# Optimization experiments

Hardware: AMD Instinct MI355X
Metric: run time of the kernel (lower is better)

Reference implementation:

```python
import jax, jax.numpy as jnp
import numpy as np

B, S, D = 2, 2048, 1024
H, HD, R = 16, 64, 128
BLOCK, TOPK = 64, 4
ROPE_BASE = 100000.0
NEG = -1e30  # finite large-negative instead of -inf to avoid NaN rows


def _rope_tables(seq_len, dim, dtype):
    inv_freq = 1.0 / (ROPE_BASE ** (jnp.arange(0, dim, 2, dtype=jnp.float32) / dim))
    freqs = jnp.arange(seq_len, dtype=jnp.float32)[:, None] * inv_freq[None, :]  # [S, dim/2]
    emb = jnp.concatenate([freqs, freqs], axis=-1)  # [S, dim]
    return jnp.cos(emb).astype(dtype), jnp.sin(emb).astype(dtype)


def _rotate_half(t):
    t1, t2 = jnp.split(t, 2, axis=-1)
    return jnp.concatenate([-t2, t1], axis=-1)


def _apply_rope(t, cos, sin):
    # t: [B, H, S, HD]; cos/sin: [S, HD]
    return t * cos[None, None] + _rotate_half(t) * sin[None, None]


def setup_inputs() -> dict:
    key = jax.random.key(0)
    ks = jax.random.split(key, 6)
    s = 0.02
    return {
        "x": jax.random.normal(ks[0], (B, S, D), jnp.float32),
        "w_q": jax.random.normal(ks[1], (D, D), jnp.float32) * s,
        "w_kv_down": jax.random.normal(ks[2], (R, D), jnp.float32) * s,
        "w_kv_up": jax.random.normal(ks[3], (2 * D, R), jnp.float32) * s,
        "w_out": jax.random.normal(ks[4], (D, D), jnp.float32) * s,
        "w_scorer": jax.random.normal(ks[5], (1, D), jnp.float32) * s,
    }


def reference(x, w_q, w_kv_down, w_kv_up, w_out, w_scorer):
    b, s, d = x.shape
    nb = s // BLOCK  # S divisible by block_size here

    q = (x @ w_q.T).reshape(b, s, H, HD).transpose(0, 2, 1, 3)  # [B,H,S,HD]
    latent = x @ w_kv_down.T                                      # [B,S,R]
    kv = latent @ w_kv_up.T                                       # [B,S,2D]
    k, v = jnp.split(kv, 2, axis=-1)
    k = k.reshape(b, s, H, HD).transpose(0, 2, 1, 3)
    v = v.reshape(b, s, H, HD).transpose(0, 2, 1, 3)

    cos, sin = _rope_tables(s, HD, x.dtype)
    q = _apply_rope(q, cos, sin)
    k = _apply_rope(k, cos, sin)

    # block relevance scores from mean-pooled block reps of x
    block_reps = x.reshape(b, nb, BLOCK, d).mean(axis=2)          # [B,nb,D]
    block_scores = (block_reps @ w_scorer.T)[..., 0]              # [B,nb]
    _, top_idx = jax.lax.top_k(block_scores, min(TOPK, nb))       # [B,topk]

    # sparse key mask: True where key position lies in a selected block
    sel = jnp.zeros((b, nb), dtype=bool)
    sel = sel.at[jnp.arange(b)[:, None], top_idx].set(True)       # [B,nb]
    sparse_mask = jnp.repeat(sel, BLOCK, axis=1)                  # [B,S]

    causal = jnp.tril(jnp.ones((s, s), dtype=bool))               # True = allowed
    allowed = sparse_mask[:, None, None, :] & causal[None, None]  # [B,1,S,S]

    scale = 1.0 / jnp.sqrt(jnp.asarray(HD, x.dtype))
    scores = jnp.einsum("bhqd,bhkd->bhqk", q, k) * scale          # [B,H,S,S]
    scores = jnp.where(allowed, scores, NEG)
    attn = jax.nn.softmax(scores, axis=-1)
    out = jnp.einsum("bhqk,bhkd->bhqd", attn, v)                  # [B,H,S,HD]
    out = out.transpose(0, 2, 1, 3).reshape(b, s, d)
    return out @ w_out.T
```

## Files before the change

### kernel.cpp

```cpp
#include <hip/hip_runtime.h>
#include <hip/hip_bf16.h>
#include <math.h>

#define B_ 2
#define S_ 2048
#define D_ 1024
#define H_ 16
#define HD_ 64
#define R_ 128
#define NBLK 32
#define TOPK_ 4
#define BS_ (B_*S_)

typedef __attribute__((ext_vector_type(8))) short bf16x8;
typedef __attribute__((ext_vector_type(4))) float f32x4;

__device__ __forceinline__ unsigned short f2bf(float f) {
    unsigned int u = __float_as_uint(f);
    u += 0x7fffu + ((u >> 16) & 1u);
    return (unsigned short)(u >> 16);
}
__device__ __forceinline__ float bf2f(unsigned short h) {
    return __uint_as_float(((unsigned int)h) << 16);
}
__device__ __forceinline__ unsigned int pack2(float a, float b) {
    return (unsigned int)f2bf(a) | ((unsigned int)f2bf(b) << 16);
}
__device__ __forceinline__ void gload_lds16(const void* g, void* l) {
    __builtin_amdgcn_global_load_lds((const __attribute__((address_space(1))) void*)g,
                                     (__attribute__((address_space(3))) void*)l, 16, 0, 0);
}

__global__ __launch_bounds__(256) void prep_k(const float* __restrict__ x,
        const float* __restrict__ wsc, const float* __restrict__ wq,
        const float* __restrict__ wkd, const float* __restrict__ wku,
        const float* __restrict__ wo, float* __restrict__ cosT,
        float* __restrict__ sinT, unsigned short* __restrict__ wcat,
        unsigned short* __restrict__ wkub, unsigned short* __restrict__ wob,
        float* __restrict__ rows, unsigned short* __restrict__ xb) {
    const int blk = blockIdx.x;
    if (blk < 512) {
        const int idx = blk*256 + threadIdx.x;
        const int s  = idx >> 6;
        const int hd = idx & 63;
        const int j = (hd < 32) ? hd : hd - 32;
        const float inv = powf(100000.0f, -((float)(2*j) / 64.0f));
        const float fr = (float)s * inv;
        cosT[idx] = cosf(fr);
        sinT[idx] = sinf(fr);
    } else if (blk < 1728) {
        const int wb = blk - 512;
        const float* src; unsigned short* dst; int base;
        if      (wb < 512) { src = wq;  dst = wcat;            base = wb;       }
        else if (wb < 576) { src = wkd; dst = wcat + 1048576;  base = wb - 512; }
        else if (wb < 704) { src = wku; dst = wkub;            base = wb - 576; }
        else               { src = wo;  dst = wob;             base = wb - 704; }
        const int i = base*2048 + threadIdx.x*8;
        float4 a = *(const float4*)&src[i];
        float4 b = *(const float4*)&src[i+4];
        uint4 o;
        o.x = pack2(a.x, a.y); o.y = pack2(a.z, a.w);
        o.z = pack2(b.x, b.y); o.w = pack2(b.z, b.w);
        *(uint4*)&dst[i] = o;
    } else {
        const int wid  = ((blk - 1728) << 2) + (threadIdx.x >> 6);
        const int lane = threadIdx.x & 63;
        #pragma unroll
        for (int r = 0; r < 4; ++r) {
            const int row = (wid << 2) + r;
            const float* xp = x + (size_t)row * D_;
            unsigned short* xo = xb + (size_t)row * D_;
            float acc = 0.f;
            #pragma unroll
            for (int j = 0; j < 4; ++j) {
                const int off = ((j << 6) + lane) << 2;
                float4 xv = *(const float4*)&xp[off];
                float4 wv = *(const float4*)&wsc[off];
                acc = fmaf(xv.x, wv.x, acc);
                acc = fmaf(xv.y, wv.y, acc);
                acc = fmaf(xv.z, wv.z, acc);
                acc = fmaf(xv.w, wv.w, acc);
                uint2 o; o.x = pack2(xv.x, xv.y); o.y = pack2(xv.z, xv.w);
                *(uint2*)&xo[off] = o;
            }
            #pragma unroll
            for (int m = 1; m <= 32; m <<= 1) acc += __shfl_xor(acc, m);
            if (lane == 0) rows[row] = acc;
        }
    }
}

__global__ __launch_bounds__(256) void blocktopk_k(const float* __restrict__ rows,
        int* __restrict__ sel, float* __restrict__ vsum) {
    ((float4*)vsum)[threadIdx.x]       = (float4){0.f,0.f,0.f,0.f};
    ((float4*)vsum)[threadIdx.x + 256] = (float4){0.f,0.f,0.f,0.f};
    __shared__ float bs[64];
    const int bk = threadIdx.x >> 2, qt = threadIdx.x & 3;
    const float* rp = rows + (bk << 6) + (qt << 4);
    float p = 0.f;
    #pragma unroll
    for (int i = 0; i < 16; ++i) p += rp[i];
    p += __shfl_xor(p, 1);
    p += __shfl_xor(p, 2);
    if (qt == 0) bs[bk] = p;
    __syncthreads();
    if (threadIdx.x < B_) {
        const int b = threadIdx.x;
        float sc[NBLK];
        for (int i = 0; i < NBLK; ++i) sc[i] = bs[b * NBLK + i];
        for (int j = 0; j < TOPK_; ++j) {
            float best = -INFINITY; int bi = 0;
            for (int i = 0; i < NBLK; ++i)
                if (sc[i] > best) { best = sc[i]; bi = i; }
            sel[b * TOPK_ + j] = bi;
            sc[bi] = -INFINITY;
        }
    }
}

template<int EPI>
__global__ __launch_bounds__(256) void gemm_mfma_k(const unsigned short* __restrict__ A,
        const unsigned short* __restrict__ Bm, int M, int N, int K,
        void* __restrict__ o0, void* __restrict__ o1,
        const float* __restrict__ cosT, const float* __restrict__ sinT,
        float* __restrict__ vsum) {
    __shared__ unsigned short shbuf[2][12288];
    const int tid  = threadIdx.x;
    const int wave = tid >> 6, lane = tid & 63;
    const int nx = N >> 6;
    const int ob = blockIdx.x;
    const int w  = ((ob & 7) * (gridDim.x >> 3)) + (ob >> 3);
    const int bm = (w / nx) << 7, bn = (w % nx) << 6;
    const int g  = lane >> 4, qc = lane & 15;
    const int srow  = lane >> 3;
    const int sslot = (lane & 7) ^ srow;

    f32x4 acc[2][4];
    #pragma unroll
    for (int m=0;m<2;m++)
        #pragma unroll
        for (int n=0;n<4;n++)
            acc[m][n] = (f32x4){0.f,0.f,0.f,0.f};

    const int NT = K >> 6;
    auto STAGE = [&](int buf, int t) {
        const int k0 = t << 6;
        unsigned short* As = shbuf[buf];
        unsigned short* Bs = shbuf[buf] + 8192;
        #pragma unroll
        for (int it = 0; it < 4; ++it) {
            const int chunk = (it << 2) | wave;
            const int row   = (chunk << 3) | srow;
            gload_lds16(A + (size_t)(bm + row) * K + k0 + (sslot << 3), &As[chunk << 9]);
        }
        #pragma unroll
        for (int it = 0; it < 2; ++it) {
            const int chunk = (it << 2) | wave;
            const int row   = (chunk << 3) | srow;
            gload_lds16(Bm + (size_t)(bn + row) * K + k0 + (sslot << 3), &Bs[chunk << 9]);
        }
    };

    STAGE(0, 0);
    __syncthreads();
    for (int t = 0; t < NT; ++t) {
        if (t + 1 < NT) STAGE((t + 1) & 1, t + 1);
        const unsigned short* As = shbuf[t & 1];
        const unsigned short* Bs = shbuf[t & 1] + 8192;
        #pragma unroll
        for (int ks = 0; ks < 2; ++ks) {
            const int swb = ((ks << 2) | g) ^ (lane & 7);
            bf16x8 af[2], bfr[4];
            #pragma unroll
            for (int m = 0; m < 2; ++m)
                af[m]  = *(const bf16x8*)&As[(((wave << 5) + (m << 4) + qc) << 6) + (swb << 3)];
            #pragma unroll
            for (int n = 0; n < 4; ++n)
                bfr[n] = *(const bf16x8*)&Bs[(((n << 4) + qc) << 6) + (swb << 3)];
            #pragma unroll
            for (int m = 0; m < 2; ++m)
                #pragma unroll
                for (int n = 0; n < 4; ++n)
                    acc[m][n] = __builtin_amdgcn_mfma_f32_16x16x32_bf16(af[m], bfr[n], acc[m][n], 0, 0, 0);
        }
        __syncthreads();
    }

    if (EPI == 0) {
        float* C = (float*)o0;
        #pragma unroll
        for (int m = 0; m < 2; ++m) {
            const int r0 = bm + (wave << 5) + (m << 4) + (g << 2);
            #pragma unroll
            for (int n = 0; n < 4; ++n) {
                const int c = bn + (n << 4) + qc;
                #pragma unroll
                for (int j = 0; j < 4; ++j)
                    C[(size_t)(r0 + j) * N + c] = acc[m][n][j];
            }
        }
    } else {
        const bool isrope = (bn < 1024);
        if (isrope) {
            const int h = bn >> 6;
            unsigned short* dst = (unsigned short*)o0;
            #pragma unroll
            for (int m = 0; m < 2; ++m) {
                const int r0 = bm + (wave << 5) + (m << 4) + (g << 2);
                #pragma unroll
                for (int j = 0; j < 4; ++j) {
                    const int row = r0 + j;
                    const int b = row >> 11, s = row & (S_-1);
                    const size_t obase = ((size_t)(b*H_ + h) * S_ + s) << 6;
                    #pragma unroll
                    for (int n = 0; n < 4; ++n) {
                        const int hd = (n << 4) + qc;
                        const float c_ = cosT[(s << 6) + hd];
                        const float sn = sinT[(s << 6) + hd];
                        const float rot = (n < 2) ? -acc[m][n ^ 2][j] : acc[m][n ^ 2][j];
                        dst[obase + hd] = f2bf(acc[m][n][j] * c_ + rot * sn);
                    }
                }
            }
        } else if (EPI == 1) {
            unsigned short* latb = (unsigned short*)o1;
            const int c0 = bn - 1024;
            #pragma unroll
            for (int m = 0; m < 2; ++m) {
                const int r0 = bm + (wave << 5) + (m << 4) + (g << 2);
                #pragma unroll
                for (int n = 0; n < 4; ++n) {
                    const int c = c0 + (n << 4) + qc;
                    #pragma unroll
                    for (int j = 0; j < 4; ++j)
                        latb[(size_t)(r0 + j) * R_ + c] = f2bf(acc[m][n][j]);
                }
            }
        } else {
            const int h  = (bn >> 6) - 16;
            const int b  = bm >> 11, s0 = bm & (S_-1);
            const int bh = (b << 4) + h;
            unsigned short* vtb = (unsigned short*)o1;
            unsigned short (*T)[72] = (unsigned short(*)[72])&shbuf[0][0];
            #pragma unroll
            for (int m = 0; m < 2; ++m) {
                const int r0 = (wave << 5) + (m << 4) + (g << 2);
                #pragma unroll
                for (int n = 0; n < 4; ++n)
                    #pragma unroll
                    for (int j = 0; j < 4; ++j)
                        T[r0 + j][(n << 4) + qc] = f2bf(acc[m][n][j]);
            }
            __syncthreads();
            #pragma unroll
            for (int u = 0; u < 2; ++u) {
                const int kb = (s0 >> 6) + u;
                unsigned short* dst = vtb + (((size_t)(bh * NBLK + kb)) << 12);
                #pragma unroll
                for (int uu = 0; uu < 2; ++uu) {
                    const int idx = (uu << 8) + tid;
                    const int dd = idx >> 3, k0 = (idx & 7) << 3;
                    unsigned short tmp[8];
                    float sm = 0.f;
                    #pragma unroll
                    for (int j = 0; j < 8; ++j) { tmp[j] = T[(u << 6) + k0 + j][dd]; sm += bf2f(tmp[j]); }
                    *(uint4*)&dst[(size_t)(dd << 6) + k0] = *(uint4*)tmp;
                    sm += __shfl_xor(sm, 1);
                    sm += __shfl_xor(sm, 2);
                    sm += __shfl_xor(sm, 4);
                    if ((tid & 7) == 0) atomicAdd(&vsum[(bh << 6) + dd], sm);
                }
            }
        }
    }
}

__global__ __launch_bounds__(256) void attn_mfma_k(const unsigned short* __restrict__ qrb,
        const unsigned short* __restrict__ krb, const unsigned short* __restrict__ vtb,
        const int* __restrict__ sel, const float* __restrict__ vsum,
        unsigned short* __restrict__ attno) {
    const int qb = blockIdx.x & (NBLK-1);
    const int bh = blockIdx.x >> 5;
    const int b  = bh >> 4;
    const int h  = bh & 15;
    const int tid  = threadIdx.x;
    const int wave = tid >> 6, lane = tid & 63;
    const int g = lane >> 4, qc = lane & 15;

    __shared__ unsigned short Ks[64*64];
    __shared__ unsigned short Vt[64*64];
    __shared__ unsigned short Pl[4][16][72];
    __shared__ float cfl[4][16];
    __shared__ float lvl[4][16];

    int selb[4];
    #pragma unroll
    for (int j=0;j<4;j++) selb[j] = sel[(b<<2)+j];
    const bool diag = (selb[0]==qb)|(selb[1]==qb)|(selb[2]==qb)|(selb[3]==qb);

    int kbl[5]; int cnt = 0;
    #pragma unroll
    for (int j=0;j<4;j++) if (selb[j] < qb) kbl[cnt++] = selb[j];
    const int dstart = cnt;
    if (diag) kbl[cnt++] = qb;

    const unsigned short* qp = qrb + (((size_t)bh*S_ + (qb<<6) + (wave<<4) + qc) << 6);
    bf16x8 bq[2];
    bq[0] = *(const bf16x8*)(qp + (g<<3));
    bq[1] = *(const bf16x8*)(qp + 32 + (g<<3));

    f32x4 oacc[4];
    #pragma unroll
    for (int n=0;n<4;n++) oacc[n] = (f32x4){0.f,0.f,0.f,0.f};
    float mrun = -INFINITY, lrun = 0.f;
    const int qib = (wave<<4) + qc;

    const int srow = lane >> 3;
    const int sslot = (lane & 7) ^ srow;

    for (int i = 0; i < cnt; ++i) {
        const int kb = kbl[i];
        const bool isdiag = (i >= dstart);
        const unsigned short* kB = krb + (((size_t)bh*S_ + (kb<<6)) << 6);
        const unsigned short* vT = vtb + (((size_t)(bh*NBLK + kb)) << 12);
        __syncthreads();
        #pragma unroll
        for (int it = 0; it < 2; ++it) {
            const int chunk = (it << 2) | wave;
            const int row = (chunk << 3) | srow;
            gload_lds16(kB + (row << 6) + (sslot << 3), &Ks[chunk << 9]);
            gload_lds16(vT + (row << 6) + (sslot << 3), &Vt[chunk << 9]);
        }
        __syncthreads();

        f32x4 sf[4];
        #pragma unroll
        for (int m=0;m<4;m++) sf[m] = (f32x4){0.f,0.f,0.f,0.f};
        #pragma unroll
        for (int ks=0;ks<2;ks++)
            #pragma unroll
            for (int m=0;m<4;m++) {
                const int sw = (((ks<<2)|g) ^ (qc & 7)) << 3;
                bf16x8 ak = *(const bf16x8*)&Ks[(((m<<4)+qc)<<6) + sw];
                sf[m] = __builtin_amdgcn_mfma_f32_16x16x32_bf16(ak, bq[ks], sf[m], 0, 0, 0);
            }

        float s[16];
        float bmax = -INFINITY;
        #pragma unroll
        for (int m=0;m<4;m++)
            #pragma unroll
            for (int r2=0;r2<4;r2++) {
                const int kl = (m<<4)+(g<<2)+r2;
                float v = sf[m][r2]*0.125f;
                if (isdiag && kl > qib) v = -1e30f;
                s[(m<<2)+r2] = v;
                bmax = fmaxf(bmax, v);
            }
        bmax = fmaxf(bmax, __shfl_xor(bmax, 16));
        bmax = fmaxf(bmax, __shfl_xor(bmax, 32));
        const float mnew = fmaxf(mrun, bmax);
        const float cf = __expf(mrun - mnew);
        float ls = 0.f;
        #pragma unroll
        for (int m=0;m<4;m++) {
            float p0 = __expf(s[(m<<2)+0]-mnew);
            float p1 = __expf(s[(m<<2)+1]-mnew);
            float p2 = __expf(s[(m<<2)+2]-mnew);
            float p3 = __expf(s[(m<<2)+3]-mnew);
            ls += p0+p1+p2+p3;
            const int koff = (m<<4)+(g<<2);
            *(unsigned int*)&Pl[wave][qc][koff]   = pack2(p0,p1);
            *(unsigned int*)&Pl[wave][qc][koff+2] = pack2(p2,p3);
        }
        ls += __shfl_xor(ls, 16);
        ls += __shfl_xor(ls, 32);
        lrun = lrun*cf + ls;
        cfl[wave][qc] = cf;
        f32x4 cf4 = *(const f32x4*)&cfl[wave][g<<2];
        #pragma unroll
        for (int n=0;n<4;n++) oacc[n] *= cf4;
        #pragma unroll
        for (int ks=0;ks<2;ks++) {
            bf16x8 pa = *(const bf16x8*)&Pl[wave][qc][(ks<<5)+(g<<3)];
            #pragma unroll
            for (int n=0;n<4;n++) {
                const int sw = (((ks<<2)|g) ^ (qc & 7)) << 3;
                bf16x8 vb = *(const bf16x8*)&Vt[(((n<<4)+qc)<<6) + sw];
                oacc[n] = __builtin_amdgcn_mfma_f32_16x16x32_bf16(pa, vb, oacc[n], 0, 0, 0);
            }
        }
        mrun = mnew;
    }

    f32x4 il4 = (f32x4){0.f,0.f,0.f,0.f};
    if (cnt) {
        lvl[wave][qc] = 1.0f / lrun;
        il4 = *(const f32x4*)&lvl[wave][g<<2];
    }
    #pragma unroll
    for (int n=0;n<4;n++)
        #pragma unroll
        for (int r2=0;r2<4;r2++) {
            float val = cnt ? oacc[n][r2]*il4[r2]
                            : vsum[(bh<<6)+(n<<4)+qc] * (1.0f/(float)S_);
            const int row = (qb<<6) + (wave<<4) + (g<<2) + r2;
            attno[(((size_t)(b*S_+row))<<10) + (h<<6) + (n<<4) + qc] = f2bf(val);
        }
}

extern "C" void kernel_launch(void* const* d_in, const int* in_sizes, int n_in,
                              void* d_out, int out_size, void* d_ws, size_t ws_size,
                              hipStream_t stream) {
    (void)in_sizes; (void)n_in; (void)out_size; (void)ws_size;
    const float* x     = (const float*)d_in[0];
    const float* w_q   = (const float*)d_in[1];
    const float* w_kvd = (const float*)d_in[2];
    const float* w_kvu = (const float*)d_in[3];
    const float* w_o   = (const float*)d_in[4];
    const float* w_sc  = (const float*)d_in[5];
    float* out = (float*)d_out;

    char* p = (char*)d_ws;
    auto alloc = [&](size_t bytes) -> void* {
        void* r = (void*)p;
        p += (bytes + 255) & ~(size_t)255;
        return r;
    };
    float* cosT  = (float*)alloc((size_t)S_*HD_*4);
    float* sinT  = (float*)alloc((size_t)S_*HD_*4);
    unsigned short* xb    = (unsigned short*)alloc((size_t)BS_*D_*2);
    unsigned short* wcat  = (unsigned short*)alloc((size_t)(D_+R_)*D_*2);
    unsigned short* wkub  = (unsigned short*)alloc((size_t)2*D_*R_*2);
    unsigned short* wob   = (unsigned short*)alloc((size_t)D_*D_*2);
    unsigned short* latb  = (unsigned short*)alloc((size_t)BS_*R_*2);
    unsigned short* qrb   = (unsigned short*)alloc((size_t)BS_*D_*2);
    unsigned short* krb   = (unsigned short*)alloc((size_t)BS_*D_*2);
    unsigned short* vtb   = (unsigned short*)alloc((size_t)BS_*D_*2);
    unsigned short* attnob= (unsigned short*)alloc((size_t)BS_*D_*2);
    float* rows   = (float*)alloc((size_t)BS_*4);
    int*   sel    = (int*)  alloc((size_t)B_*TOPK_*4);
    float* vsum   = (float*)alloc((size_t)B_*H_*HD_*4);

    prep_k<<<1984, 256, 0, stream>>>(x, w_sc, w_q, w_kvd, w_kvu, w_o,
                                     cosT, sinT, wcat, wkub, wob, rows, xb);
    blocktopk_k<<<1, 256, 0, stream>>>(rows, sel, vsum);

    gemm_mfma_k<1><<<576, 256, 0, stream>>>(
        xb, wcat, BS_, D_+R_, D_, qrb, latb, cosT, sinT, nullptr);
    gemm_mfma_k<2><<<1024, 256, 0, stream>>>(
        latb, wkub, BS_, 2*D_, R_, krb, vtb, cosT, sinT, vsum);

    attn_mfma_k<<<B_*H_*NBLK, 256, 0, stream>>>(qrb, krb, vtb, sel, vsum, attnob);
    gemm_mfma_k<0><<<512, 256, 0, stream>>>(
        attnob, wob, BS_, D_, D_, out, nullptr, nullptr, nullptr, nullptr);
}
```

Baseline: 143.0 us.

## Double-buffer K tiles in LDS and load V directly into registers

Replaces the single K/V LDS staging with a two-slot K buffer that prefetches the next selected key block while the current one is being computed. V is read directly from global memory into registers instead of going through LDS. The per-row rescale factors are broadcast with lane shuffles rather than through shared scratch, and MFMA sections are wrapped in s_setprio. This hides global load latency and trims LDS traffic, at the cost of more register pressure and uncoalesced-ish direct V loads. The kernel only processes up to five blocks per workgroup, so there is limited overlap to gain.

```diff
diff --git a/kernel.cpp b/kernel.cpp
--- a/kernel.cpp
+++ b/kernel.cpp
@@ -287,11 +287,8 @@
     const int wave = tid >> 6, lane = tid & 63;
     const int g = lane >> 4, qc = lane & 15;
 
-    __shared__ unsigned short Ks[64*64];
-    __shared__ unsigned short Vt[64*64];
+    __shared__ unsigned short Ks[2][4096];
     __shared__ unsigned short Pl[4][16][72];
-    __shared__ float cfl[4][16];
-    __shared__ float lvl[4][16];
 
     int selb[4];
     #pragma unroll
@@ -318,32 +315,46 @@
     const int srow = lane >> 3;
     const int sslot = (lane & 7) ^ srow;
 
-    for (int i = 0; i < cnt; ++i) {
-        const int kb = kbl[i];
-        const bool isdiag = (i >= dstart);
+    auto stageK = [&](int buf, int kb) {
         const unsigned short* kB = krb + (((size_t)bh*S_ + (kb<<6)) << 6);
-        const unsigned short* vT = vtb + (((size_t)(bh*NBLK + kb)) << 12);
-        __syncthreads();
         #pragma unroll
         for (int it = 0; it < 2; ++it) {
             const int chunk = (it << 2) | wave;
             const int row = (chunk << 3) | srow;
-            gload_lds16(kB + (row << 6) + (sslot << 3), &Ks[chunk << 9]);
-            gload_lds16(vT + (row << 6) + (sslot << 3), &Vt[chunk << 9]);
-        }
-        __syncthreads();
+            gload_lds16(kB + (row << 6) + (sslot << 3), &Ks[buf][chunk << 9]);
+        }
+    };
+
+    if (cnt) stageK(0, kbl[0]);
+    __syncthreads();
+
+    for (int i = 0; i < cnt; ++i) {
+        const int cur = i & 1;
+        if (i + 1 < cnt) stageK(cur ^ 1, kbl[i + 1]);
+        const int kb = kbl[i];
+        const bool isdiag = (i >= dstart);
+
+        const unsigned short* vT = vtb + (((size_t)(bh*NBLK + kb)) << 12);
+        bf16x8 vb[2][4];
+        #pragma unroll
+        for (int ks=0;ks<2;ks++)
+            #pragma unroll
+            for (int n=0;n<4;n++)
+                vb[ks][n] = *(const bf16x8*)(vT + (((n<<4)+qc)<<6) + (ks<<5) + (g<<3));
 
         f32x4 sf[4];
         #pragma unroll
         for (int m=0;m<4;m++) sf[m] = (f32x4){0.f,0.f,0.f,0.f};
+        __builtin_amdgcn_s_setprio(1);
         #pragma unroll
         for (int ks=0;ks<2;ks++)
             #pragma unroll
             for (int m=0;m<4;m++) {
                 const int sw = (((ks<<2)|g) ^ (qc & 7)) << 3;
-                bf16x8 ak = *(const bf16x8*)&Ks[(((m<<4)+qc)<<6) + sw];
+                bf16x8 ak = *(const bf16x8*)&Ks[cur][(((m<<4)+qc)<<6) + sw];
                 sf[m] = __builtin_amdgcn_mfma_f32_16x16x32_bf16(ak, bq[ks], sf[m], 0, 0, 0);
             }
+        __builtin_amdgcn_s_setprio(0);
 
         float s[16];
         float bmax = -INFINITY;
@@ -376,27 +387,29 @@
         ls += __shfl_xor(ls, 16);
         ls += __shfl_xor(ls, 32);
         lrun = lrun*cf + ls;
-        cfl[wave][qc] = cf;
-        f32x4 cf4 = *(const f32x4*)&cfl[wave][g<<2];
+        f32x4 cf4;
+        #pragma unroll
+        for (int j=0;j<4;j++) cf4[j] = __shfl(cf, (g<<2)+j);
         #pragma unroll
         for (int n=0;n<4;n++) oacc[n] *= cf4;
+        __builtin_amdgcn_s_setprio(1);
         #pragma unroll
         for (int ks=0;ks<2;ks++) {
             bf16x8 pa = *(const bf16x8*)&Pl[wave][qc][(ks<<5)+(g<<3)];
             #pragma unroll
-            for (int n=0;n<4;n++) {
-                const int sw = (((ks<<2)|g) ^ (qc & 7)) << 3;
-                bf16x8 vb = *(const bf16x8*)&Vt[(((n<<4)+qc)<<6) + sw];
-                oacc[n] = __builtin_amdgcn_mfma_f32_16x16x32_bf16(pa, vb, oacc[n], 0, 0, 0);
-            }
-        }
+            for (int n=0;n<4;n++)
+                oacc[n] = __builtin_amdgcn_mfma_f32_16x16x32_bf16(pa, vb[ks][n], oacc[n], 0, 0, 0);
+        }
+        __builtin_amdgcn_s_setprio(0);
         mrun = mnew;
+        __syncthreads();
     }
 
     f32x4 il4 = (f32x4){0.f,0.f,0.f,0.f};
     if (cnt) {
-        lvl[wave][qc] = 1.0f / lrun;
-        il4 = *(const f32x4*)&lvl[wave][g<<2];
+        const float il = 1.0f / lrun;
+        #pragma unroll
+        for (int j=0;j<4;j++) il4[j] = __shfl(il, (g<<2)+j);
     }
     #pragma unroll
     for (int n=0;n<4;n++)
```

New measurement: 153.9 us. 7.6% more time.
